# Kernel tuning notes

Hardware: AMD Instinct MI355X
Metric: run time of the kernel (lower is better)

Reference implementation:

```python
import jax, jax.numpy as jnp
import numpy as np

# Graph sizes
B, N, E = 8, 512, 262144          # graphs, nodes/graph, total edges
ND, ED, GD = 128, 64, 32          # node, edge, glob feature dims
FIN = 2 * ND + ED                 # 320 = msg('sr') + existing edges
CTX = GD                          # ctxt_dim = 0, ctxt is globs only
H1, OUT = 256, 64                 # feat_net hidden / output (== ED for 'add' residual)
AH, NHEADS = 64, 4                # attn_net hidden / heads
HEAD = OUT // NHEADS              # 16
EPS = 1e-5


def setup_inputs() -> dict:
    key = jax.random.key(0)
    ks = jax.random.split(key, 12)
    nodes = jax.random.normal(ks[0], (B, N, ND), jnp.float32)
    edges0 = jax.random.normal(ks[1], (E, ED), jnp.float32)
    globs = jax.random.normal(ks[2], (B, GD), jnp.float32)
    batch_idx = jnp.sort(jax.random.randint(ks[3], (E,), 0, B, jnp.int32))
    send_idx = jax.random.randint(ks[4], (E,), 0, N, jnp.int32)
    recv_idx = jax.random.randint(ks[5], (E,), 0, N, jnp.int32)
    # LayerNorm params over feat_inpt_dim
    ln_g = jnp.ones((FIN,), jnp.float32)
    ln_b = jnp.zeros((FIN,), jnp.float32)
    # feat_net: 2-layer SiLU MLP, ctxt concatenated at the input
    W1 = 0.05 * jax.random.normal(ks[6], (FIN + CTX, H1), jnp.float32)
    b1 = jnp.zeros((H1,), jnp.float32)
    W2 = 0.05 * jax.random.normal(ks[7], (H1, OUT), jnp.float32)
    b2 = jnp.zeros((OUT,), jnp.float32)
    # attn_net: 2-layer SiLU MLP -> n_heads scores
    A1 = 0.05 * jax.random.normal(ks[8], (FIN + CTX, AH), jnp.float32)
    ab1 = jnp.zeros((AH,), jnp.float32)
    A2 = 0.05 * jax.random.normal(ks[9], (AH, NHEADS), jnp.float32)
    ab2 = jnp.zeros((NHEADS,), jnp.float32)
    return dict(nodes=nodes, edges0=edges0, globs=globs, ln_g=ln_g, ln_b=ln_b,
                W1=W1, b1=b1, W2=W2, b2=b2, A1=A1, ab1=ab1, A2=A2, ab2=ab2,
                batch_idx=batch_idx, send_idx=send_idx, recv_idx=recv_idx)


def reference(nodes, edges0, globs, ln_g, ln_b, W1, b1, W2, b2, A1, ab1, A2, ab2,
              batch_idx, send_idx, recv_idx):
    # Build messages: gather sender/receiver node feats per edge ('sr')
    send = nodes[batch_idx, send_idx]                      # [E, ND]
    recv = nodes[batch_idx, recv_idx]                      # [E, ND]
    feats = jnp.concatenate([edges0, send, recv], axis=-1)  # [E, FIN]
    # Pre-LN
    mu = feats.mean(-1, keepdims=True)
    var = feats.var(-1, keepdims=True)
    feats = (feats - mu) * jax.lax.rsqrt(var + EPS) * ln_g + ln_b
    # Broadcast per-graph globals to edges (ctxt_from_mask)
    x = jnp.concatenate([feats, globs[batch_idx]], axis=-1)  # [E, FIN+CTX]
    # Attention scores / sqrt(feat_outp_dim)
    a = (jax.nn.silu(x @ A1 + ab1) @ A2 + ab2) / np.sqrt(OUT)  # [E, NHEADS]
    # Segment softmax over the sender dim (group by (graph, receiver))
    seg = batch_idx * N + recv_idx
    nseg = B * N
    amax = jax.ops.segment_max(a, seg, num_segments=nseg)
    amax = jnp.where(jnp.isfinite(amax), amax, 0.0)
    ae = jnp.exp(a - amax[seg])
    denom = jax.ops.segment_sum(ae, seg, num_segments=nseg)
    attn = ae / denom[seg]                                  # [E, NHEADS]
    attn = jnp.repeat(attn, HEAD, axis=-1)                  # [E, OUT]
    # Edge feature update + additive residual
    new_edges = jax.nn.silu(x @ W1 + b1) @ W2 + b2 + edges0  # [E, OUT]
    # Attention-weighted scatter-sum pool over senders, zeros for isolated nodes
    pooled = jax.ops.segment_sum(new_edges * attn, seg, num_segments=nseg)
    pooled = pooled.reshape(B, N, OUT)
    return new_edges, pooled
```

## Files before the change

kernel.cpp:

```cpp
#include <hip/hip_runtime.h>
#include <hip/hip_bf16.h>
#include <cstdint>

typedef __bf16 bf16;
typedef __bf16 bf16x8 __attribute__((ext_vector_type(8)));
typedef float f32x4 __attribute__((ext_vector_type(4)));
typedef unsigned int u32;

#define E_TOT   262144
#define NNODE   512
#define NDIM    128
#define EDIM    64
#define GDIM    32
#define FIN     320
#define XD      352
#define H1D     256
#define OUTD    64
#define AHD     64
#define NHEADS  4
#define NSEG    4096
#define TE      48
#define CAP     192

#define SX_STR  360
#define SH_STR  264
#define SA_STR  72

#define PRM_LNG 0
#define PRM_LNB 320
#define PRM_B1  640
#define PRM_B2  896
#define PRM_A2  960
#define PRM_AB1 1216
#define PRM_AB2 1280
#define PRM_TOT 1284

#define SMEM_SX    0
#define SMEM_SA    25600
#define SMEM_A2    34560
#define SMEM_LNG   35584
#define SMEM_LNB   36864
#define SMEM_IDX   38144
#define SMEM_TOT   38720

#define SOFF 510

__device__ __forceinline__ float siluf(float v) {
    return v / (1.0f + __expf(-v));
}

__device__ __forceinline__ float ldf(const void* p, size_t i, bool isb) {
    return isb ? (float)((const bf16*)p)[i] : ((const float*)p)[i];
}

__device__ __forceinline__ bool probe_bf16(const void* nodes, int t) {
    const unsigned short* u16 = (const unsigned short*)nodes;
    int lane = t & 63;
    int pl = 0;
    #pragma unroll
    for (int i = 0; i < 4; i++) {
        unsigned short u = u16[lane * 4 + i];
        int expo = (u >> 7) & 0xFF;
        pl += (((u & 0x7FFF) == 0) || (expo >= 97 && expo <= 137)) ? 1 : 0;
    }
    #pragma unroll
    for (int m = 1; m < 64; m <<= 1) pl += __shfl_xor(pl, m);
    return pl >= 240;
}

__global__ __launch_bounds__(256) void k_prep(
    const void* __restrict__ nodes,
    const void* __restrict__ W1, const void* __restrict__ W2, const void* __restrict__ A1,
    const void* __restrict__ ln_g, const void* __restrict__ ln_b,
    const void* __restrict__ b1, const void* __restrict__ b2,
    const void* __restrict__ A2, const void* __restrict__ ab1, const void* __restrict__ ab2,
    const int* __restrict__ bidx, const int* __restrict__ ridx,
    bf16* __restrict__ W1T, bf16* __restrict__ W2T, bf16* __restrict__ A1T,
    float* __restrict__ prm, u32* __restrict__ cnt, u32* __restrict__ order) {
    int b = blockIdx.x, t = threadIdx.x;
    if (b >= SOFF) {
        int ge = (b - SOFF) * 256 + t;
        int seg = bidx[ge] * NNODE + ridx[ge];
        u32 pos = atomicAdd(&cnt[seg], 1u);
        if (pos < CAP) order[(size_t)seg * CAP + pos] = (u32)ge;
        return;
    }
    bool isb = probe_bf16(nodes, t);
    if (b < 352) {
        int i = b * 256 + t;
        int k = i / H1D, n = i % H1D;
        float v = isb ? (float)((const bf16*)W1)[i] : ((const float*)W1)[i];
        W1T[n * XD + k] = (bf16)v;
    } else if (b < 416) {
        int i = (b - 352) * 256 + t;
        int k = i / OUTD, n = i % OUTD;
        float v = isb ? (float)((const bf16*)W2)[i] : ((const float*)W2)[i];
        W2T[n * H1D + k] = (bf16)v;
    } else if (b < 504) {
        int i = (b - 416) * 256 + t;
        int k = i / AHD, n = i % AHD;
        float v = isb ? (float)((const bf16*)A1)[i] : ((const float*)A1)[i];
        A1T[n * XD + k] = (bf16)v;
    } else {
        int i = (b - 504) * 256 + t;
        if (i < PRM_TOT) {
            const void* src; int off;
            if (i < 320)       { src = ln_g; off = i; }
            else if (i < 640)  { src = ln_b; off = i - 320; }
            else if (i < 896)  { src = b1;   off = i - 640; }
            else if (i < 960)  { src = b2;   off = i - 896; }
            else if (i < 1216) { src = A2;   off = i - 960; }
            else if (i < 1280) { src = ab1;  off = i - 1216; }
            else               { src = ab2;  off = i - 1280; }
            prm[i] = isb ? (float)((const bf16*)src)[off] : ((const float*)src)[off];
        }
    }
}

__global__ __launch_bounds__(256, 4) void k_edge(
    const void* __restrict__ nodes, const void* __restrict__ edges0,
    const void* __restrict__ globs, const float* __restrict__ prm,
    const int* __restrict__ bidx, const int* __restrict__ sidx,
    const int* __restrict__ ridx,
    const bf16* __restrict__ W1T, const bf16* __restrict__ W2T,
    const bf16* __restrict__ A1T,
    void* __restrict__ outNE, float* __restrict__ scrS) {

    __shared__ __align__(16) char smem[SMEM_TOT];
    bf16*  sX    = (bf16*)(smem + SMEM_SX);
    bf16*  sH    = (bf16*)(smem + SMEM_SX);
    bf16*  sA    = (bf16*)(smem + SMEM_SA);
    float* sA2   = (float*)(smem + SMEM_A2);
    float* sLnG  = (float*)(smem + SMEM_LNG);
    float* sLnB  = (float*)(smem + SMEM_LNB);
    int*   sBi   = (int*)(smem + SMEM_IDX);
    int*   sSi   = sBi + TE;
    int*   sRi   = sBi + 2 * TE;

    const int t  = threadIdx.x;
    const int e0 = blockIdx.x * TE;
    const int ne = min(TE, E_TOT - e0);
    const bool isb = probe_bf16(nodes, t);

    if (t < TE) {
        int ge = e0 + t;
        if (t < ne) {
            sBi[t] = bidx[ge]; sSi[t] = sidx[ge]; sRi[t] = ridx[ge];
        } else {
            sBi[t] = 0; sSi[t] = 0; sRi[t] = 0;
        }
    } else if (t < 128) {
        int c = t - 48;
        if (c < 80) ((float4*)sLnG)[c] = ((const float4*)(prm + PRM_LNG))[c];
    } else if (t < 208) {
        int c = t - 128;
        ((float4*)sLnB)[c] = ((const float4*)(prm + PRM_LNB))[c];
    } else {
        int c = t - 208;
        if (c < 32) {
            ((float4*)sA2)[c]      = ((const float4*)(prm + PRM_A2))[c];
            ((float4*)sA2)[c + 32] = ((const float4*)(prm + PRM_A2))[c + 32];
        }
    }
    __syncthreads();

    {
        const int eh = t >> 3, gl = t & 7;
        for (int half = 0; half < 2; half++) {
            const int e = half * 32 + eh;
            if (e >= TE) break;
            if (e >= ne) {
                bf16x8 zz = {};
                #pragma unroll
                for (int j = 0; j < 6; j++) {
                    int c = gl + j * 8;
                    if (c < 44) *(bf16x8*)&sX[e * SX_STR + c * 8] = zz;
                }
                continue;
            }
            const int ge = e0 + e;
            const int bi = sBi[e], si = sSi[e], ri = sRi[e];
            float v[40];
            #pragma unroll
            for (int j = 0; j < 5; j++) {
                const int c = gl + j * 8;
                const void* base; size_t off;
                if (c < 8)       { base = edges0; off = (size_t)ge * EDIM + c * 8; }
                else if (c < 24) { base = nodes;  off = (size_t)(bi * NNODE + si) * NDIM + (c - 8) * 8; }
                else             { base = nodes;  off = (size_t)(bi * NNODE + ri) * NDIM + (c - 24) * 8; }
                if (isb) {
                    bf16x8 x = *(const bf16x8*)((const bf16*)base + off);
                    #pragma unroll
                    for (int ii = 0; ii < 8; ii++) v[j * 8 + ii] = (float)x[ii];
                } else {
                    const float* sf = (const float*)base + off;
                    float4 f0 = ((const float4*)sf)[0];
                    float4 f1 = ((const float4*)sf)[1];
                    v[j*8+0]=f0.x; v[j*8+1]=f0.y; v[j*8+2]=f0.z; v[j*8+3]=f0.w;
                    v[j*8+4]=f1.x; v[j*8+5]=f1.y; v[j*8+6]=f1.z; v[j*8+7]=f1.w;
                }
            }
            float s = 0.f, sq = 0.f;
            #pragma unroll
            for (int ii = 0; ii < 40; ii++) { s += v[ii]; sq += v[ii] * v[ii]; }
            #pragma unroll
            for (int m = 1; m < 8; m <<= 1) { s += __shfl_xor(s, m); sq += __shfl_xor(sq, m); }
            float mean = s * (1.0f / FIN);
            float var  = sq * (1.0f / FIN) - mean * mean;
            float rstd = rsqrtf(var + 1e-5f);
            #pragma unroll
            for (int j = 0; j < 5; j++) {
                const int c = gl + j * 8;
                const float* gP = &sLnG[c * 8];
                const float* bP = &sLnB[c * 8];
                bf16x8 o;
                #pragma unroll
                for (int ii = 0; ii < 8; ii++)
                    o[ii] = (bf16)((v[j * 8 + ii] - mean) * rstd * gP[ii] + bP[ii]);
                *(bf16x8*)&sX[e * SX_STR + c * 8] = o;
            }
            if (gl < 4) {
                const int c = 40 + gl;
                size_t off = (size_t)bi * GDIM + gl * 8;
                bf16x8 o;
                if (isb) {
                    o = *(const bf16x8*)((const bf16*)globs + off);
                } else {
                    const float* sf = (const float*)globs + off;
                    float4 f0 = ((const float4*)sf)[0];
                    float4 f1 = ((const float4*)sf)[1];
                    o[0]=(bf16)f0.x; o[1]=(bf16)f0.y; o[2]=(bf16)f0.z; o[3]=(bf16)f0.w;
                    o[4]=(bf16)f1.x; o[5]=(bf16)f1.y; o[6]=(bf16)f1.z; o[7]=(bf16)f1.w;
                }
                *(bf16x8*)&sX[e * SX_STR + c * 8] = o;
            }
        }
    }
    __syncthreads();

    const int w = t >> 6, lane = t & 63, quad = lane >> 4, l15 = lane & 15;
    f32x4 z = {0.f, 0.f, 0.f, 0.f};

    f32x4 acc[3][4], accA[3];
    #pragma unroll
    for (int s2 = 0; s2 < 3; s2++) { accA[s2] = z; for (int i = 0; i < 4; i++) acc[s2][i] = z; }
    {
        const bf16* pW = W1T + (size_t)(w * 64 + l15) * XD + quad * 8;
        const bf16* pA = A1T + (size_t)(w * 16 + l15) * XD + quad * 8;
        bf16x8 bw[4], ba;
        #pragma unroll
        for (int i = 0; i < 4; i++) bw[i] = *(const bf16x8*)(pW + (size_t)i * 16 * XD);
        ba = *(const bf16x8*)pA;
        #pragma unroll 1
        for (int kk = 0; kk < 11; kk++) {
            bf16x8 bwn[4], ban;
            if (kk < 10) {
                #pragma unroll
                for (int i = 0; i < 4; i++) bwn[i] = *(const bf16x8*)(pW + (size_t)i * 16 * XD + (kk + 1) * 32);
                ban = *(const bf16x8*)(pA + (kk + 1) * 32);
            }
            const int kc = kk * 32 + quad * 8;
            bf16x8 a[3];
            #pragma unroll
            for (int s2 = 0; s2 < 3; s2++) a[s2] = *(bf16x8*)&sX[(s2 * 16 + l15) * SX_STR + kc];
            #pragma unroll
            for (int i = 0; i < 4; i++)
                #pragma unroll
                for (int s2 = 0; s2 < 3; s2++)
                    acc[s2][i] = __builtin_amdgcn_mfma_f32_16x16x32_bf16(a[s2], bw[i], acc[s2][i], 0, 0, 0);
            #pragma unroll
            for (int s2 = 0; s2 < 3; s2++)
                accA[s2] = __builtin_amdgcn_mfma_f32_16x16x32_bf16(a[s2], ba, accA[s2], 0, 0, 0);
            if (kk < 10) {
                #pragma unroll
                for (int i = 0; i < 4; i++) bw[i] = bwn[i];
                ba = ban;
            }
        }
    }
    __syncthreads();

    #pragma unroll
    for (int i = 0; i < 4; i++) {
        const int n = w * 64 + i * 16 + l15;
        const float bb = prm[PRM_B1 + n];
        #pragma unroll
        for (int s2 = 0; s2 < 3; s2++)
            #pragma unroll
            for (int r = 0; r < 4; r++)
                sH[(s2 * 16 + quad * 4 + r) * SH_STR + n] = (bf16)siluf(acc[s2][i][r] + bb);
    }
    {
        const int n = w * 16 + l15;
        const float ba1 = prm[PRM_AB1 + n];
        #pragma unroll
        for (int s2 = 0; s2 < 3; s2++)
            #pragma unroll
            for (int r = 0; r < 4; r++)
                sA[(s2 * 16 + quad * 4 + r) * SA_STR + n] = (bf16)siluf(accA[s2][r] + ba1);
    }
    __syncthreads();

    if (t < TE * NHEADS) {
        const int e = t >> 2, h = t & 3;
        if (e < ne) {
            float dot = 0.f;
            #pragma unroll
            for (int c = 0; c < 8; c++) {
                bf16x8 vv = *(bf16x8*)&sA[e * SA_STR + c * 8];
                #pragma unroll
                for (int ii = 0; ii < 8; ii++)
                    dot += (float)vv[ii] * sA2[(c * 8 + ii) * NHEADS + h];
            }
            scrS[(size_t)(e0 + e) * NHEADS + h] = __expf((dot + prm[PRM_AB2 + h]) * 0.125f);
        }
    }

    {
        f32x4 c2[3] = {z, z, z};
        const int n = w * 16 + l15;
        const bf16* pW2 = W2T + (size_t)n * H1D + quad * 8;
        bf16x8 b2f = *(const bf16x8*)pW2;
        #pragma unroll 1
        for (int kk = 0; kk < 8; kk++) {
            bf16x8 b2n;
            if (kk < 7) b2n = *(const bf16x8*)(pW2 + (kk + 1) * 32);
            const int kc = kk * 32 + quad * 8;
            #pragma unroll
            for (int s2 = 0; s2 < 3; s2++) {
                bf16x8 a = *(bf16x8*)&sH[(s2 * 16 + l15) * SH_STR + kc];
                c2[s2] = __builtin_amdgcn_mfma_f32_16x16x32_bf16(a, b2f, c2[s2], 0, 0, 0);
            }
            if (kk < 7) b2f = b2n;
        }
        const float bb2 = prm[PRM_B2 + n];
        #pragma unroll
        for (int s2 = 0; s2 < 3; s2++)
            #pragma unroll
            for (int r = 0; r < 4; r++) {
                const int row = s2 * 16 + quad * 4 + r;
                if (row < ne) {
                    size_t off = (size_t)(e0 + row) * EDIM + n;
                    float ev = isb ? (float)((const bf16*)edges0)[off] : ((const float*)edges0)[off];
                    float v = c2[s2][r] + bb2 + ev;
                    if (isb) ((bf16*)outNE)[off] = (bf16)v;
                    else     ((float*)outNE)[off] = v;
                }
            }
    }
}

__global__ __launch_bounds__(256) void k_pool(const u32* __restrict__ cnt,
                                              const u32* __restrict__ order,
                                              const float* __restrict__ scrS,
                                              const void* __restrict__ nodes,
                                              void* __restrict__ d_out) {
    const int t = threadIdx.x;
    const bool isb = probe_bf16(nodes, t);
    const int ws = blockIdx.x * 4 + (t >> 6);
    const int lane = t & 63, h = lane >> 4;
    const void* newE = d_out;

    const u32 n1 = min(cnt[ws], (u32)CAP);
    const u32 base = (u32)ws * CAP;
    float acc = 0.f, dsum = 0.f;
    u32 i = 0;
    for (; i + 4 <= n1; i += 4) {
        u32 ea = order[base + i], eb = order[base + i + 1];
        u32 ec = order[base + i + 2], ed = order[base + i + 3];
        float sa = scrS[(size_t)ea * NHEADS + h];
        float sb = scrS[(size_t)eb * NHEADS + h];
        float sc = scrS[(size_t)ec * NHEADS + h];
        float sd = scrS[(size_t)ed * NHEADS + h];
        float va = ldf(newE, (size_t)ea * EDIM + lane, isb);
        float vb = ldf(newE, (size_t)eb * EDIM + lane, isb);
        float vc = ldf(newE, (size_t)ec * EDIM + lane, isb);
        float vd = ldf(newE, (size_t)ed * EDIM + lane, isb);
        acc += va * sa + vb * sb + vc * sc + vd * sd;
        dsum += sa + sb + sc + sd;
    }
    for (; i < n1; i++) {
        u32 e = order[base + i];
        float s = scrS[(size_t)e * NHEADS + h];
        acc += ldf(newE, (size_t)e * EDIM + lane, isb) * s;
        dsum += s;
    }
    float r = (dsum > 0.f) ? acc / dsum : 0.f;
    size_t po = (size_t)E_TOT * OUTD + (size_t)ws * OUTD + lane;
    if (isb) ((bf16*)d_out)[po] = (bf16)r;
    else     ((float*)d_out)[po] = r;
}

static char* align_up(char* p, size_t a) {
    return (char*)(((uintptr_t)p + (a - 1)) & ~(uintptr_t)(a - 1));
}

extern "C" void kernel_launch(void* const* d_in, const int* in_sizes, int n_in,
                              void* d_out, int out_size, void* d_ws, size_t ws_size,
                              hipStream_t stream) {
    const void* nodes  = d_in[0];
    const void* edges0 = d_in[1];
    const void* globs  = d_in[2];
    const void* ln_g   = d_in[3];
    const void* ln_b   = d_in[4];
    const void* W1     = d_in[5];
    const void* b1     = d_in[6];
    const void* W2     = d_in[7];
    const void* b2     = d_in[8];
    const void* A1     = d_in[9];
    const void* ab1    = d_in[10];
    const void* A2     = d_in[11];
    const void* ab2    = d_in[12];
    const int*  bidx   = (const int*)d_in[13];
    const int*  sidx   = (const int*)d_in[14];
    const int*  ridx   = (const int*)d_in[15];

    char* p = (char*)d_ws;
    float* prm    = (float*)p;  p = align_up(p + PRM_TOT * 4, 256);
    bf16*  W1T    = (bf16*)p;   p = align_up(p + XD * H1D * 2, 256);
    bf16*  W2T    = (bf16*)p;   p = align_up(p + H1D * OUTD * 2, 256);
    bf16*  A1T    = (bf16*)p;   p = align_up(p + XD * AHD * 2, 256);
    u32*   cnt    = (u32*)p;    p += NSEG * 4;
    u32*   order  = (u32*)p;    p += (size_t)NSEG * CAP * 4;
    float* scrS   = (float*)p;  p += (size_t)E_TOT * NHEADS * 4;

    hipMemsetAsync(cnt, 0, NSEG * 4, stream);
    k_prep<<<dim3(SOFF + E_TOT / 256), dim3(256), 0, stream>>>(
        nodes, W1, W2, A1, ln_g, ln_b, b1, b2, A2, ab1, ab2,
        bidx, ridx, W1T, W2T, A1T, prm, cnt, order);
    k_edge<<<dim3((E_TOT + TE - 1) / TE), dim3(256), 0, stream>>>(
        nodes, edges0, globs, prm,
        bidx, sidx, ridx, W1T, W2T, A1T, d_out, scrS);
    k_pool<<<dim3(NSEG / 4), dim3(256), 0, stream>>>(cnt, order, scrS, nodes, d_out);
}
```

Before: 333.0 us.

## Precompute per-node and per-graph first-layer projections, folding LayerNorm algebraically

The per-edge first layer (K=352) is factored by linearity. LayerNorm is folded into the weights as rstd*(x·gW - mu*sum(gW)) + ln_b·W. The sender, receiver and global contributions are precomputed once per node and per graph in k_prep, along with per-node sum and sum-of-squares stats. The edge kernel then runs MFMA only over the 64 edge features and adds gathered fp32 table rows. This removes most of the per-edge GEMM work and the node-feature gathers, at the cost of large fp32 table gathers (4096x256 per table) per edge row, a heavier prep kernel, and numerical differences from the mean-subtraction reformulation.

```diff
diff --git a/kernel.cpp b/kernel.cpp
--- a/kernel.cpp
+++ b/kernel.cpp
@@ -13,18 +13,17 @@
 #define EDIM    64
 #define GDIM    32
 #define FIN     320
-#define XD      352
 #define H1D     256
 #define OUTD    64
 #define AHD     64
 #define NHEADS  4
 #define NSEG    4096
+#define NND     4096
 #define TE      48
 #define CAP     192
 
-#define SX_STR  360
+#define SX_STR  72
 #define SH_STR  264
-#define SA_STR  72
 
 #define PRM_LNG 0
 #define PRM_LNB 320
@@ -35,15 +34,23 @@
 #define PRM_AB2 1280
 #define PRM_TOT 1284
 
-#define SMEM_SX    0
-#define SMEM_SA    25600
-#define SMEM_A2    34560
-#define SMEM_LNG   35584
-#define SMEM_LNB   36864
-#define SMEM_IDX   38144
-#define SMEM_TOT   38720
-
-#define SOFF 510
+#define SMEM_SH    0
+#define SMEM_SX    25600
+#define SMEM_MU    32512
+#define SMEM_A2    32896
+#define SMEM_IDX   33920
+#define SMEM_TOT   34496
+
+#define KP_W1E   0
+#define KP_A1E   64
+#define KP_W2T   80
+#define KP_PRM   144
+#define KP_GL    150
+#define KP_GC    158
+#define KP_GCA   159
+#define KP_TAB   160
+#define KP_SCAT  672
+#define KP_NBLK  1696
 
 __device__ __forceinline__ float siluf(float v) {
     return v / (1.0f + __expf(-v));
@@ -69,40 +76,48 @@
 }
 
 __global__ __launch_bounds__(256) void k_prep(
-    const void* __restrict__ nodes,
+    const void* __restrict__ nodes, const void* __restrict__ globs,
     const void* __restrict__ W1, const void* __restrict__ W2, const void* __restrict__ A1,
     const void* __restrict__ ln_g, const void* __restrict__ ln_b,
     const void* __restrict__ b1, const void* __restrict__ b2,
     const void* __restrict__ A2, const void* __restrict__ ab1, const void* __restrict__ ab2,
     const int* __restrict__ bidx, const int* __restrict__ ridx,
-    bf16* __restrict__ W1T, bf16* __restrict__ W2T, bf16* __restrict__ A1T,
-    float* __restrict__ prm, u32* __restrict__ cnt, u32* __restrict__ order) {
+    bf16* __restrict__ W1eT, bf16* __restrict__ A1eT, bf16* __restrict__ W2T,
+    float* __restrict__ prm,
+    float* __restrict__ Gvec, float* __restrict__ Cvec,
+    float* __restrict__ GAv,  float* __restrict__ CAv,
+    float* __restrict__ Gltab, float* __restrict__ GlAtab,
+    float2* __restrict__ SQ,
+    float* __restrict__ Stab, float* __restrict__ Rtab,
+    float* __restrict__ SAtab, float* __restrict__ RAtab,
+    u32* __restrict__ cnt, u32* __restrict__ order) {
+
+    __shared__ float sNd[1024];
     int b = blockIdx.x, t = threadIdx.x;
-    if (b >= SOFF) {
-        int ge = (b - SOFF) * 256 + t;
+
+    if (b >= KP_SCAT) {
+        int ge = (b - KP_SCAT) * 256 + t;
         int seg = bidx[ge] * NNODE + ridx[ge];
         u32 pos = atomicAdd(&cnt[seg], 1u);
         if (pos < CAP) order[(size_t)seg * CAP + pos] = (u32)ge;
         return;
     }
     bool isb = probe_bf16(nodes, t);
-    if (b < 352) {
+
+    if (b < KP_A1E) {
         int i = b * 256 + t;
-        int k = i / H1D, n = i % H1D;
-        float v = isb ? (float)((const bf16*)W1)[i] : ((const float*)W1)[i];
-        W1T[n * XD + k] = (bf16)v;
-    } else if (b < 416) {
-        int i = (b - 352) * 256 + t;
-        int k = i / OUTD, n = i % OUTD;
-        float v = isb ? (float)((const bf16*)W2)[i] : ((const float*)W2)[i];
-        W2T[n * H1D + k] = (bf16)v;
-    } else if (b < 504) {
-        int i = (b - 416) * 256 + t;
-        int k = i / AHD, n = i % AHD;
-        float v = isb ? (float)((const bf16*)A1)[i] : ((const float*)A1)[i];
-        A1T[n * XD + k] = (bf16)v;
-    } else {
-        int i = (b - 504) * 256 + t;
+        int n = i >> 6, k = i & 63;
+        W1eT[i] = (bf16)(ldf(ln_g, k, isb) * ldf(W1, (size_t)k * H1D + n, isb));
+    } else if (b < KP_W2T) {
+        int i = (b - KP_A1E) * 256 + t;
+        int n = i >> 6, k = i & 63;
+        A1eT[i] = (bf16)(ldf(ln_g, k, isb) * ldf(A1, (size_t)k * AHD + n, isb));
+    } else if (b < KP_PRM) {
+        int i = (b - KP_W2T) * 256 + t;
+        int k = i >> 6, n = i & 63;
+        W2T[n * H1D + k] = (bf16)ldf(W2, i, isb);
+    } else if (b < KP_GL) {
+        int i = (b - KP_PRM) * 256 + t;
         if (i < PRM_TOT) {
             const void* src; int off;
             if (i < 320)       { src = ln_g; off = i; }
@@ -112,30 +127,121 @@
             else if (i < 1216) { src = A2;   off = i - 960; }
             else if (i < 1280) { src = ab1;  off = i - 1216; }
             else               { src = ab2;  off = i - 1280; }
-            prm[i] = isb ? (float)((const bf16*)src)[off] : ((const float*)src)[off];
+            prm[i] = ldf(src, off, isb);
+        }
+    } else if (b < KP_GC) {
+        int bg = b - KP_GL;
+        float acc = 0.f;
+        #pragma unroll 4
+        for (int k = 0; k < GDIM; k++)
+            acc += ldf(globs, bg * GDIM + k, isb) * ldf(W1, (size_t)(FIN + k) * H1D + t, isb);
+        Gltab[bg * H1D + t] = acc;
+        if (t < AHD) {
+            float a2 = 0.f;
+            #pragma unroll 4
+            for (int k = 0; k < GDIM; k++)
+                a2 += ldf(globs, bg * GDIM + k, isb) * ldf(A1, (size_t)(FIN + k) * AHD + t, isb);
+            GlAtab[bg * AHD + t] = a2;
+        }
+    } else if (b < KP_GCA) {
+        float g = 0.f, c = ldf(b1, t, isb);
+        #pragma unroll 4
+        for (int k = 0; k < FIN; k++) {
+            float wv = ldf(W1, (size_t)k * H1D + t, isb);
+            g += ldf(ln_g, k, isb) * wv;
+            c += ldf(ln_b, k, isb) * wv;
+        }
+        Gvec[t] = g; Cvec[t] = c;
+    } else if (b < KP_TAB) {
+        if (t < AHD) {
+            float g = 0.f, c = ldf(ab1, t, isb);
+            #pragma unroll 4
+            for (int k = 0; k < FIN; k++) {
+                float wv = ldf(A1, (size_t)k * AHD + t, isb);
+                g += ldf(ln_g, k, isb) * wv;
+                c += ldf(ln_b, k, isb) * wv;
+            }
+            GAv[t] = g; CAv[t] = c;
+        }
+    } else {
+        int v0 = (b - KP_TAB) * 8;
+        #pragma unroll
+        for (int q = 0; q < 4; q++)
+            sNd[t + q * 256] = ldf(nodes, (size_t)v0 * NDIM + t + q * 256, isb);
+        __syncthreads();
+        {
+            int nj = t >> 5, li = t & 31;
+            float s = 0.f, qq = 0.f;
+            #pragma unroll
+            for (int m = 0; m < 4; m++) {
+                float x = sNd[nj * NDIM + li + m * 32];
+                s += x; qq += x * x;
+            }
+            #pragma unroll
+            for (int m = 1; m < 32; m <<= 1) { s += __shfl_xor(s, m); qq += __shfl_xor(qq, m); }
+            if (li == 0) SQ[v0 + nj] = make_float2(s, qq);
+        }
+        {
+            float aS[8] = {}, aR[8] = {};
+            for (int k = 0; k < NDIM; k++) {
+                float wS = ldf(ln_g, EDIM + k, isb) * ldf(W1, (size_t)(EDIM + k) * H1D + t, isb);
+                float wR = ldf(ln_g, EDIM + NDIM + k, isb) * ldf(W1, (size_t)(EDIM + NDIM + k) * H1D + t, isb);
+                #pragma unroll
+                for (int j = 0; j < 8; j++) {
+                    aS[j] += sNd[j * NDIM + k] * wS;
+                    aR[j] += sNd[j * NDIM + k] * wR;
+                }
+            }
+            #pragma unroll
+            for (int j = 0; j < 8; j++) {
+                Stab[(size_t)(v0 + j) * H1D + t] = aS[j];
+                Rtab[(size_t)(v0 + j) * H1D + t] = aR[j];
+            }
+        }
+        if (t < AHD) {
+            float aS[8] = {}, aR[8] = {};
+            for (int k = 0; k < NDIM; k++) {
+                float wS = ldf(ln_g, EDIM + k, isb) * ldf(A1, (size_t)(EDIM + k) * AHD + t, isb);
+                float wR = ldf(ln_g, EDIM + NDIM + k, isb) * ldf(A1, (size_t)(EDIM + NDIM + k) * AHD + t, isb);
+                #pragma unroll
+                for (int j = 0; j < 8; j++) {
+                    aS[j] += sNd[j * NDIM + k] * wS;
+                    aR[j] += sNd[j * NDIM + k] * wR;
+                }
+            }
+            #pragma unroll
+            for (int j = 0; j < 8; j++) {
+                SAtab[(size_t)(v0 + j) * AHD + t] = aS[j];
+                RAtab[(size_t)(v0 + j) * AHD + t] = aR[j];
+            }
         }
     }
 }
 
 __global__ __launch_bounds__(256, 4) void k_edge(
     const void* __restrict__ nodes, const void* __restrict__ edges0,
-    const void* __restrict__ globs, const float* __restrict__ prm,
+    const float* __restrict__ prm,
     const int* __restrict__ bidx, const int* __restrict__ sidx,
     const int* __restrict__ ridx,
-    const bf16* __restrict__ W1T, const bf16* __restrict__ W2T,
-    const bf16* __restrict__ A1T,
+    const bf16* __restrict__ W1eT, const bf16* __restrict__ A1eT,
+    const bf16* __restrict__ W2T,
+    const float* __restrict__ Gvec, const float* __restrict__ Cvec,
+    const float* __restrict__ GAv,  const float* __restrict__ CAv,
+    const float* __restrict__ Gltab, const float* __restrict__ GlAtab,
+    const float2* __restrict__ SQ,
+    const float* __restrict__ Stab, const float* __restrict__ Rtab,
+    const float* __restrict__ SAtab, const float* __restrict__ RAtab,
     void* __restrict__ outNE, float* __restrict__ scrS) {
 
     __shared__ __align__(16) char smem[SMEM_TOT];
-    bf16*  sX    = (bf16*)(smem + SMEM_SX);
-    bf16*  sH    = (bf16*)(smem + SMEM_SX);
-    bf16*  sA    = (bf16*)(smem + SMEM_SA);
-    float* sA2   = (float*)(smem + SMEM_A2);
-    float* sLnG  = (float*)(smem + SMEM_LNG);
-    float* sLnB  = (float*)(smem + SMEM_LNB);
-    int*   sBi   = (int*)(smem + SMEM_IDX);
-    int*   sSi   = sBi + TE;
-    int*   sRi   = sBi + 2 * TE;
+    bf16*   sH   = (bf16*)(smem + SMEM_SH);
+    bf16*   sX   = (bf16*)(smem + SMEM_SX);
+    bf16*   sA   = (bf16*)(smem + SMEM_SX);
+    float2* sMu  = (float2*)(smem + SMEM_MU);
+    float*  sA2  = (float*)(smem + SMEM_A2);
+    int*    sBi  = (int*)(smem + SMEM_IDX);
+    int*    sNs  = sBi + TE;
+    int*    sNr  = sBi + 2 * TE;
 
     const int t  = threadIdx.x;
     const int e0 = blockIdx.x * TE;
@@ -144,23 +250,14 @@
 
     if (t < TE) {
         int ge = e0 + t;
-        if (t < ne) {
-            sBi[t] = bidx[ge]; sSi[t] = sidx[ge]; sRi[t] = ridx[ge];
-        } else {
-            sBi[t] = 0; sSi[t] = 0; sRi[t] = 0;
-        }
-    } else if (t < 128) {
-        int c = t - 48;
-        if (c < 80) ((float4*)sLnG)[c] = ((const float4*)(prm + PRM_LNG))[c];
-    } else if (t < 208) {
-        int c = t - 128;
-        ((float4*)sLnB)[c] = ((const float4*)(prm + PRM_LNB))[c];
-    } else {
-        int c = t - 208;
-        if (c < 32) {
-            ((float4*)sA2)[c]      = ((const float4*)(prm + PRM_A2))[c];
-            ((float4*)sA2)[c + 32] = ((const float4*)(prm + PRM_A2))[c + 32];
-        }
+        int bi = 0, si = 0, ri = 0;
+        if (t < ne) { bi = bidx[ge]; si = sidx[ge]; ri = ridx[ge]; }
+        int ns = bi * NNODE + si, nr = bi * NNODE + ri;
+        sBi[t] = bi; sNs[t] = ns; sNr[t] = nr;
+        float2 a = SQ[ns], c = SQ[nr];
+        sMu[t] = make_float2(a.x + c.x, a.y + c.y);
+    } else if (t >= 64 && t < 128) {
+        ((float4*)sA2)[t - 64] = ((const float4*)(prm + PRM_A2))[t - 64];
     }
     __syncthreads();
 
@@ -171,68 +268,38 @@
             if (e >= TE) break;
             if (e >= ne) {
                 bf16x8 zz = {};
+                *(bf16x8*)&sX[e * SX_STR + gl * 8] = zz;
+                if (gl == 0) sMu[e] = make_float2(0.f, 1.f);
+                continue;
+            }
+            const size_t off = (size_t)(e0 + e) * EDIM + gl * 8;
+            float v[8];
+            bf16x8 o;
+            if (isb) {
+                o = *(const bf16x8*)((const bf16*)edges0 + off);
                 #pragma unroll
-                for (int j = 0; j < 6; j++) {
-                    int c = gl + j * 8;
-                    if (c < 44) *(bf16x8*)&sX[e * SX_STR + c * 8] = zz;
-                }
-                continue;
-            }
-            const int ge = e0 + e;
-            const int bi = sBi[e], si = sSi[e], ri = sRi[e];
-            float v[40];
-            #pragma unroll
-            for (int j = 0; j < 5; j++) {
-                const int c = gl + j * 8;
-                const void* base; size_t off;
-                if (c < 8)       { base = edges0; off = (size_t)ge * EDIM + c * 8; }
-                else if (c < 24) { base = nodes;  off = (size_t)(bi * NNODE + si) * NDIM + (c - 8) * 8; }
-                else             { base = nodes;  off = (size_t)(bi * NNODE + ri) * NDIM + (c - 24) * 8; }
-                if (isb) {
-                    bf16x8 x = *(const bf16x8*)((const bf16*)base + off);
-                    #pragma unroll
-                    for (int ii = 0; ii < 8; ii++) v[j * 8 + ii] = (float)x[ii];
-                } else {
-                    const float* sf = (const float*)base + off;
-                    float4 f0 = ((const float4*)sf)[0];
-                    float4 f1 = ((const float4*)sf)[1];
-                    v[j*8+0]=f0.x; v[j*8+1]=f0.y; v[j*8+2]=f0.z; v[j*8+3]=f0.w;
-                    v[j*8+4]=f1.x; v[j*8+5]=f1.y; v[j*8+6]=f1.z; v[j*8+7]=f1.w;
-                }
-            }
+                for (int ii = 0; ii < 8; ii++) v[ii] = (float)o[ii];
+            } else {
+                const float* sf = (const float*)edges0 + off;
+                float4 f0 = ((const float4*)sf)[0];
+                float4 f1 = ((const float4*)sf)[1];
+                v[0]=f0.x; v[1]=f0.y; v[2]=f0.z; v[3]=f0.w;
+                v[4]=f1.x; v[5]=f1.y; v[6]=f1.z; v[7]=f1.w;
+                #pragma unroll
+                for (int ii = 0; ii < 8; ii++) o[ii] = (bf16)v[ii];
+            }
+            *(bf16x8*)&sX[e * SX_STR + gl * 8] = o;
             float s = 0.f, sq = 0.f;
             #pragma unroll
-            for (int ii = 0; ii < 40; ii++) { s += v[ii]; sq += v[ii] * v[ii]; }
+            for (int ii = 0; ii < 8; ii++) { s += v[ii]; sq += v[ii] * v[ii]; }
             #pragma unroll
             for (int m = 1; m < 8; m <<= 1) { s += __shfl_xor(s, m); sq += __shfl_xor(sq, m); }
-            float mean = s * (1.0f / FIN);
-            float var  = sq * (1.0f / FIN) - mean * mean;
-            float rstd = rsqrtf(var + 1e-5f);
-            #pragma unroll
-            for (int j = 0; j < 5; j++) {
-                const int c = gl + j * 8;
-                const float* gP = &sLnG[c * 8];
-                const float* bP = &sLnB[c * 8];
-                bf16x8 o;
-                #pragma unroll
-                for (int ii = 0; ii < 8; ii++)
-                    o[ii] = (bf16)((v[j * 8 + ii] - mean) * rstd * gP[ii] + bP[ii]);
-                *(bf16x8*)&sX[e * SX_STR + c * 8] = o;
-            }
-            if (gl < 4) {
-                const int c = 40 + gl;
-                size_t off = (size_t)bi * GDIM + gl * 8;
-                bf16x8 o;
-                if (isb) {
-                    o = *(const bf16x8*)((const bf16*)globs + off);
-                } else {
-                    const float* sf = (const float*)globs + off;
-                    float4 f0 = ((const float4*)sf)[0];
-                    float4 f1 = ((const float4*)sf)[1];
-                    o[0]=(bf16)f0.x; o[1]=(bf16)f0.y; o[2]=(bf16)f0.z; o[3]=(bf16)f0.w;
-                    o[4]=(bf16)f1.x; o[5]=(bf16)f1.y; o[6]=(bf16)f1.z; o[7]=(bf16)f1.w;
-                }
-                *(bf16x8*)&sX[e * SX_STR + c * 8] = o;
+            if (gl == 0) {
+                float2 nq = sMu[e];
+                float st = s + nq.x, qt = sq + nq.y;
+                float mean = st * (1.0f / FIN);
+                float var  = qt * (1.0f / FIN) - mean * mean;
+                sMu[e] = make_float2(mean, rsqrtf(var + 1e-5f));
             }
         }
     }
@@ -245,20 +312,14 @@
     #pragma unroll
     for (int s2 = 0; s2 < 3; s2++) { accA[s2] = z; for (int i = 0; i < 4; i++) acc[s2][i] = z; }
     {
-        const bf16* pW = W1T + (size_t)(w * 64 + l15) * XD + quad * 8;
-        const bf16* pA = A1T + (size_t)(w * 16 + l15) * XD + quad * 8;
-        bf16x8 bw[4], ba;
+        const bf16* pW = W1eT + (size_t)(w * 64 + l15) * EDIM + quad * 8;
+        const bf16* pA = A1eT + (size_t)(w * 16 + l15) * EDIM + quad * 8;
         #pragma unroll
-        for (int i = 0; i < 4; i++) bw[i] = *(const bf16x8*)(pW + (size_t)i * 16 * XD);
-        ba = *(const bf16x8*)pA;
-        #pragma unroll 1
-        for (int kk = 0; kk < 11; kk++) {
-            bf16x8 bwn[4], ban;
-            if (kk < 10) {
-                #pragma unroll
-                for (int i = 0; i < 4; i++) bwn[i] = *(const bf16x8*)(pW + (size_t)i * 16 * XD + (kk + 1) * 32);
-                ban = *(const bf16x8*)(pA + (kk + 1) * 32);
-            }
+        for (int kk = 0; kk < 2; kk++) {
+            bf16x8 bw[4], ba;
+            #pragma unroll
+            for (int i = 0; i < 4; i++) bw[i] = *(const bf16x8*)(pW + i * 16 * EDIM + kk * 32);
+            ba = *(const bf16x8*)(pA + kk * 32);
             const int kc = kk * 32 + quad * 8;
             bf16x8 a[3];
             #pragma unroll
@@ -271,33 +332,38 @@
             #pragma unroll
             for (int s2 = 0; s2 < 3; s2++)
                 accA[s2] = __builtin_amdgcn_mfma_f32_16x16x32_bf16(a[s2], ba, accA[s2], 0, 0, 0);
-            if (kk < 10) {
-                #pragma unroll
-                for (int i = 0; i < 4; i++) bw[i] = bwn[i];
-                ba = ban;
-            }
         }
     }
     __syncthreads();
 
-    #pragma unroll
+    #pragma unroll 1
     for (int i = 0; i < 4; i++) {
         const int n = w * 64 + i * 16 + l15;
-        const float bb = prm[PRM_B1 + n];
+        const float Gn = Gvec[n], Cn = Cvec[n];
         #pragma unroll
         for (int s2 = 0; s2 < 3; s2++)
             #pragma unroll
-            for (int r = 0; r < 4; r++)
-                sH[(s2 * 16 + quad * 4 + r) * SH_STR + n] = (bf16)siluf(acc[s2][i][r] + bb);
+            for (int r = 0; r < 4; r++) {
+                const int row = s2 * 16 + quad * 4 + r;
+                float2 mr = sMu[row];
+                float S = Stab[(size_t)sNs[row] * H1D + n] + Rtab[(size_t)sNr[row] * H1D + n];
+                float val = mr.y * (acc[s2][i][r] + S - mr.x * Gn) + Gltab[sBi[row] * H1D + n] + Cn;
+                sH[row * SH_STR + n] = (bf16)siluf(val);
+            }
     }
     {
         const int n = w * 16 + l15;
-        const float ba1 = prm[PRM_AB1 + n];
+        const float Gn = GAv[n], Cn = CAv[n];
         #pragma unroll
         for (int s2 = 0; s2 < 3; s2++)
             #pragma unroll
-            for (int r = 0; r < 4; r++)
-                sA[(s2 * 16 + quad * 4 + r) * SA_STR + n] = (bf16)siluf(accA[s2][r] + ba1);
+            for (int r = 0; r < 4; r++) {
+                const int row = s2 * 16 + quad * 4 + r;
+                float2 mr = sMu[row];
+                float S = SAtab[(size_t)sNs[row] * AHD + n] + RAtab[(size_t)sNr[row] * AHD + n];
+                float val = mr.y * (accA[s2][r] + S - mr.x * Gn) + GlAtab[sBi[row] * AHD + n] + Cn;
+                sA[row * SX_STR + n] = (bf16)siluf(val);
+            }
     }
     __syncthreads();
 
@@ -307,7 +373,7 @@
             float dot = 0.f;
             #pragma unroll
             for (int c = 0; c < 8; c++) {
-                bf16x8 vv = *(bf16x8*)&sA[e * SA_STR + c * 8];
+                bf16x8 vv = *(bf16x8*)&sA[e * SX_STR + c * 8];
                 #pragma unroll
                 for (int ii = 0; ii < 8; ii++)
                     dot += (float)vv[ii] * sA2[(c * 8 + ii) * NHEADS + h];
@@ -416,20 +482,34 @@
     const int*  ridx   = (const int*)d_in[15];
 
     char* p = (char*)d_ws;
-    float* prm    = (float*)p;  p = align_up(p + PRM_TOT * 4, 256);
-    bf16*  W1T    = (bf16*)p;   p = align_up(p + XD * H1D * 2, 256);
-    bf16*  W2T    = (bf16*)p;   p = align_up(p + H1D * OUTD * 2, 256);
-    bf16*  A1T    = (bf16*)p;   p = align_up(p + XD * AHD * 2, 256);
-    u32*   cnt    = (u32*)p;    p += NSEG * 4;
-    u32*   order  = (u32*)p;    p += (size_t)NSEG * CAP * 4;
-    float* scrS   = (float*)p;  p += (size_t)E_TOT * NHEADS * 4;
+    float*  prm    = (float*)p;   p = align_up(p + PRM_TOT * 4, 256);
+    bf16*   W1eT   = (bf16*)p;    p = align_up(p + H1D * EDIM * 2, 256);
+    bf16*   A1eT   = (bf16*)p;    p = align_up(p + AHD * EDIM * 2, 256);
+    bf16*   W2T    = (bf16*)p;    p = align_up(p + H1D * OUTD * 2, 256);
+    float*  Gvec   = (float*)p;   p += H1D * 4;
+    float*  Cvec   = (float*)p;   p += H1D * 4;
+    float*  GAv    = (float*)p;   p += AHD * 4;
+    float*  CAv    = (float*)p;   p += AHD * 4;
+    float*  Gltab  = (float*)p;   p += 8 * H1D * 4;
+    float*  GlAtab = (float*)p;   p = align_up(p + 8 * AHD * 4, 256);
+    float2* SQ     = (float2*)p;  p += (size_t)NND * 8;
+    float*  Stab   = (float*)p;   p += (size_t)NND * H1D * 4;
+    float*  Rtab   = (float*)p;   p += (size_t)NND * H1D * 4;
+    float*  SAtab  = (float*)p;   p += (size_t)NND * AHD * 4;
+    float*  RAtab  = (float*)p;   p += (size_t)NND * AHD * 4;
+    u32*    cnt    = (u32*)p;     p += NSEG * 4;
+    u32*    order  = (u32*)p;     p += (size_t)NSEG * CAP * 4;
+    float*  scrS   = (float*)p;   p += (size_t)E_TOT * NHEADS * 4;
 
     hipMemsetAsync(cnt, 0, NSEG * 4, stream);
-    k_prep<<<dim3(SOFF + E_TOT / 256), dim3(256), 0, stream>>>(
-        nodes, W1, W2, A1, ln_g, ln_b, b1, b2, A2, ab1, ab2,
-        bidx, ridx, W1T, W2T, A1T, prm, cnt, order);
+    k_prep<<<dim3(KP_NBLK), dim3(256), 0, stream>>>(
+        nodes, globs, W1, W2, A1, ln_g, ln_b, b1, b2, A2, ab1, ab2,
+        bidx, ridx, W1eT, A1eT, W2T, prm,
+        Gvec, Cvec, GAv, CAv, Gltab, GlAtab, SQ,
+        Stab, Rtab, SAtab, RAtab, cnt, order);
     k_edge<<<dim3((E_TOT + TE - 1) / TE), dim3(256), 0, stream>>>(
-        nodes, edges0, globs, prm,
-        bidx, sidx, ridx, W1T, W2T, A1T, d_out, scrS);
+        nodes, edges0, prm, bidx, sidx, ridx,
+        W1eT, A1eT, W2T, Gvec, Cvec, GAv, CAv, Gltab, GlAtab, SQ,
+        Stab, Rtab, SAtab, RAtab, d_out, scrS);
     k_pool<<<dim3(NSEG / 4), dim3(256), 0, stream>>>(cnt, order, scrS, nodes, d_out);
 }
```

Measured after the change: 576.7 us. 1.73x slower.

## Fold LayerNorm affine and normalization into GEMM epilogue via precomputed weight sums

Applied to the files above, without the earlier changes.

Precomputes gamma-scaled W1/A1 and per-output vectors G=gamma·W and C=beta·W+bias in the prep kernel. The edge kernel stores raw (unnormalized) features in shared memory and applies rstd*acc - rstd*mean*G + C in the epilogue, and scales globs by the std so they stay unnormalized. This removes per-element LayerNorm arithmetic and the ln param staging from the gather phase. Rounding raw values to bf16 before mean subtraction adds a precision risk, and the prep kernel gains atomics.

```diff
diff --git a/kernel.cpp b/kernel.cpp
--- a/kernel.cpp
+++ b/kernel.cpp
@@ -36,14 +36,19 @@
 #define PRM_TOT 1284
 
 #define SMEM_SX    0
+#define SMEM_A2    34560
+#define SMEM_IDX   35584
+#define SMEM_MU    36160
+#define SMEM_TOT   36544
 #define SMEM_SA    25600
-#define SMEM_A2    34560
-#define SMEM_LNG   35584
-#define SMEM_LNB   36864
-#define SMEM_IDX   38144
-#define SMEM_TOT   38720
-
-#define SOFF 510
+
+#define KP_W1T   0
+#define KP_W2T   352
+#define KP_A1T   416
+#define KP_PRM   504
+#define KP_GC    510
+#define KP_SCAT  550
+#define KP_NBLK  1574
 
 __device__ __forceinline__ float siluf(float v) {
     return v / (1.0f + __expf(-v));
@@ -76,33 +81,34 @@
     const void* __restrict__ A2, const void* __restrict__ ab1, const void* __restrict__ ab2,
     const int* __restrict__ bidx, const int* __restrict__ ridx,
     bf16* __restrict__ W1T, bf16* __restrict__ W2T, bf16* __restrict__ A1T,
-    float* __restrict__ prm, u32* __restrict__ cnt, u32* __restrict__ order) {
+    float* __restrict__ prm,
+    float* __restrict__ Gvec, float* __restrict__ Cvec,
+    float* __restrict__ GAv,  float* __restrict__ CAv,
+    u32* __restrict__ cnt, u32* __restrict__ order) {
     int b = blockIdx.x, t = threadIdx.x;
-    if (b >= SOFF) {
-        int ge = (b - SOFF) * 256 + t;
+    if (b >= KP_SCAT) {
+        int ge = (b - KP_SCAT) * 256 + t;
         int seg = bidx[ge] * NNODE + ridx[ge];
         u32 pos = atomicAdd(&cnt[seg], 1u);
         if (pos < CAP) order[(size_t)seg * CAP + pos] = (u32)ge;
         return;
     }
     bool isb = probe_bf16(nodes, t);
-    if (b < 352) {
-        int i = b * 256 + t;
-        int k = i / H1D, n = i % H1D;
-        float v = isb ? (float)((const bf16*)W1)[i] : ((const float*)W1)[i];
-        W1T[n * XD + k] = (bf16)v;
-    } else if (b < 416) {
-        int i = (b - 352) * 256 + t;
+    if (b < KP_W2T) {
+        int k = b, n = t;
+        float g = (k < FIN) ? ldf(ln_g, k, isb) : 1.0f;
+        W1T[n * XD + k] = (bf16)(ldf(W1, (size_t)k * H1D + n, isb) * g);
+    } else if (b < KP_A1T) {
+        int i = (b - KP_W2T) * 256 + t;
         int k = i / OUTD, n = i % OUTD;
-        float v = isb ? (float)((const bf16*)W2)[i] : ((const float*)W2)[i];
-        W2T[n * H1D + k] = (bf16)v;
-    } else if (b < 504) {
-        int i = (b - 416) * 256 + t;
-        int k = i / AHD, n = i % AHD;
-        float v = isb ? (float)((const bf16*)A1)[i] : ((const float*)A1)[i];
-        A1T[n * XD + k] = (bf16)v;
-    } else {
-        int i = (b - 504) * 256 + t;
+        W2T[n * H1D + k] = (bf16)ldf(W2, i, isb);
+    } else if (b < KP_PRM) {
+        int i = (b - KP_A1T) * 256 + t;
+        int k = i >> 6, n = i & 63;
+        float g = (k < FIN) ? ldf(ln_g, k, isb) : 1.0f;
+        A1T[n * XD + k] = (bf16)(ldf(A1, i, isb) * g);
+    } else if (b < KP_GC) {
+        int i = (b - KP_PRM) * 256 + t;
         if (i < PRM_TOT) {
             const void* src; int off;
             if (i < 320)       { src = ln_g; off = i; }
@@ -112,7 +118,33 @@
             else if (i < 1216) { src = A2;   off = i - 960; }
             else if (i < 1280) { src = ab1;  off = i - 1216; }
             else               { src = ab2;  off = i - 1280; }
-            prm[i] = isb ? (float)((const bf16*)src)[off] : ((const float*)src)[off];
+            prm[i] = ldf(src, off, isb);
+        }
+    } else {
+        int j = b - KP_GC;
+        float g = 0.f, c = 0.f;
+        #pragma unroll
+        for (int kk = 0; kk < 8; kk++) {
+            int k = j * 8 + kk;
+            float gam = ldf(ln_g, k, isb), bet = ldf(ln_b, k, isb);
+            float wv = ldf(W1, (size_t)k * H1D + t, isb);
+            g += gam * wv; c += bet * wv;
+        }
+        if (j == 0) c += ldf(b1, t, isb);
+        atomicAdd(&Gvec[t], g);
+        atomicAdd(&Cvec[t], c);
+        if (t < AHD) {
+            float gA = 0.f, cA = 0.f;
+            #pragma unroll
+            for (int kk = 0; kk < 8; kk++) {
+                int k = j * 8 + kk;
+                float wv = ldf(A1, (size_t)k * AHD + t, isb);
+                gA += ldf(ln_g, k, isb) * wv;
+                cA += ldf(ln_b, k, isb) * wv;
+            }
+            if (j == 0) cA += ldf(ab1, t, isb);
+            atomicAdd(&GAv[t], gA);
+            atomicAdd(&CAv[t], cA);
         }
     }
 }
@@ -124,18 +156,19 @@
     const int* __restrict__ ridx,
     const bf16* __restrict__ W1T, const bf16* __restrict__ W2T,
     const bf16* __restrict__ A1T,
+    const float* __restrict__ Gvec, const float* __restrict__ Cvec,
+    const float* __restrict__ GAv,  const float* __restrict__ CAv,
     void* __restrict__ outNE, float* __restrict__ scrS) {
 
     __shared__ __align__(16) char smem[SMEM_TOT];
-    bf16*  sX    = (bf16*)(smem + SMEM_SX);
-    bf16*  sH    = (bf16*)(smem + SMEM_SX);
-    bf16*  sA    = (bf16*)(smem + SMEM_SA);
-    float* sA2   = (float*)(smem + SMEM_A2);
-    float* sLnG  = (float*)(smem + SMEM_LNG);
-    float* sLnB  = (float*)(smem + SMEM_LNB);
-    int*   sBi   = (int*)(smem + SMEM_IDX);
-    int*   sSi   = sBi + TE;
-    int*   sRi   = sBi + 2 * TE;
+    bf16*   sX   = (bf16*)(smem + SMEM_SX);
+    bf16*   sH   = (bf16*)(smem + SMEM_SX);
+    bf16*   sA   = (bf16*)(smem + SMEM_SA);
+    float*  sA2  = (float*)(smem + SMEM_A2);
+    int*    sBi  = (int*)(smem + SMEM_IDX);
+    int*    sSi  = sBi + TE;
+    int*    sRi  = sBi + 2 * TE;
+    float2* sMu  = (float2*)(smem + SMEM_MU);
 
     const int t  = threadIdx.x;
     const int e0 = blockIdx.x * TE;
@@ -149,18 +182,8 @@
         } else {
             sBi[t] = 0; sSi[t] = 0; sRi[t] = 0;
         }
-    } else if (t < 128) {
-        int c = t - 48;
-        if (c < 80) ((float4*)sLnG)[c] = ((const float4*)(prm + PRM_LNG))[c];
-    } else if (t < 208) {
-        int c = t - 128;
-        ((float4*)sLnB)[c] = ((const float4*)(prm + PRM_LNB))[c];
-    } else {
-        int c = t - 208;
-        if (c < 32) {
-            ((float4*)sA2)[c]      = ((const float4*)(prm + PRM_A2))[c];
-            ((float4*)sA2)[c + 32] = ((const float4*)(prm + PRM_A2))[c + 32];
-        }
+    } else if (t >= 64 && t < 128) {
+        ((float4*)sA2)[t - 64] = ((const float4*)(prm + PRM_A2))[t - 64];
     }
     __syncthreads();
 
@@ -176,11 +199,13 @@
                     int c = gl + j * 8;
                     if (c < 44) *(bf16x8*)&sX[e * SX_STR + c * 8] = zz;
                 }
+                if (gl == 0) sMu[e] = make_float2(1.f, 0.f);
                 continue;
             }
             const int ge = e0 + e;
             const int bi = sBi[e], si = sSi[e], ri = sRi[e];
             float v[40];
+            bf16x8 xr[5];
             #pragma unroll
             for (int j = 0; j < 5; j++) {
                 const int c = gl + j * 8;
@@ -189,15 +214,17 @@
                 else if (c < 24) { base = nodes;  off = (size_t)(bi * NNODE + si) * NDIM + (c - 8) * 8; }
                 else             { base = nodes;  off = (size_t)(bi * NNODE + ri) * NDIM + (c - 24) * 8; }
                 if (isb) {
-                    bf16x8 x = *(const bf16x8*)((const bf16*)base + off);
+                    xr[j] = *(const bf16x8*)((const bf16*)base + off);
                     #pragma unroll
-                    for (int ii = 0; ii < 8; ii++) v[j * 8 + ii] = (float)x[ii];
+                    for (int ii = 0; ii < 8; ii++) v[j * 8 + ii] = (float)xr[j][ii];
                 } else {
                     const float* sf = (const float*)base + off;
                     float4 f0 = ((const float4*)sf)[0];
                     float4 f1 = ((const float4*)sf)[1];
                     v[j*8+0]=f0.x; v[j*8+1]=f0.y; v[j*8+2]=f0.z; v[j*8+3]=f0.w;
                     v[j*8+4]=f1.x; v[j*8+5]=f1.y; v[j*8+6]=f1.z; v[j*8+7]=f1.w;
+                    #pragma unroll
+                    for (int ii = 0; ii < 8; ii++) xr[j][ii] = (bf16)v[j * 8 + ii];
                 }
             }
             float s = 0.f, sq = 0.f;
@@ -208,29 +235,27 @@
             float mean = s * (1.0f / FIN);
             float var  = sq * (1.0f / FIN) - mean * mean;
             float rstd = rsqrtf(var + 1e-5f);
+            float sd   = (var + 1e-5f) * rstd;
+            if (gl == 0) sMu[e] = make_float2(rstd, -rstd * mean);
             #pragma unroll
             for (int j = 0; j < 5; j++) {
                 const int c = gl + j * 8;
-                const float* gP = &sLnG[c * 8];
-                const float* bP = &sLnB[c * 8];
-                bf16x8 o;
-                #pragma unroll
-                for (int ii = 0; ii < 8; ii++)
-                    o[ii] = (bf16)((v[j * 8 + ii] - mean) * rstd * gP[ii] + bP[ii]);
-                *(bf16x8*)&sX[e * SX_STR + c * 8] = o;
+                *(bf16x8*)&sX[e * SX_STR + c * 8] = xr[j];
             }
             if (gl < 4) {
                 const int c = 40 + gl;
                 size_t off = (size_t)bi * GDIM + gl * 8;
                 bf16x8 o;
                 if (isb) {
-                    o = *(const bf16x8*)((const bf16*)globs + off);
+                    bf16x8 gr = *(const bf16x8*)((const bf16*)globs + off);
+                    #pragma unroll
+                    for (int ii = 0; ii < 8; ii++) o[ii] = (bf16)((float)gr[ii] * sd);
                 } else {
                     const float* sf = (const float*)globs + off;
                     float4 f0 = ((const float4*)sf)[0];
                     float4 f1 = ((const float4*)sf)[1];
-                    o[0]=(bf16)f0.x; o[1]=(bf16)f0.y; o[2]=(bf16)f0.z; o[3]=(bf16)f0.w;
-                    o[4]=(bf16)f1.x; o[5]=(bf16)f1.y; o[6]=(bf16)f1.z; o[7]=(bf16)f1.w;
+                    o[0]=(bf16)(f0.x*sd); o[1]=(bf16)(f0.y*sd); o[2]=(bf16)(f0.z*sd); o[3]=(bf16)(f0.w*sd);
+                    o[4]=(bf16)(f1.x*sd); o[5]=(bf16)(f1.y*sd); o[6]=(bf16)(f1.z*sd); o[7]=(bf16)(f1.w*sd);
                 }
                 *(bf16x8*)&sX[e * SX_STR + c * 8] = o;
             }
@@ -280,24 +305,32 @@
     }
     __syncthreads();
 
-    #pragma unroll
+    #pragma unroll 1
     for (int i = 0; i < 4; i++) {
         const int n = w * 64 + i * 16 + l15;
-        const float bb = prm[PRM_B1 + n];
+        const float Gn = Gvec[n], Cn = Cvec[n];
         #pragma unroll
         for (int s2 = 0; s2 < 3; s2++)
             #pragma unroll
-            for (int r = 0; r < 4; r++)
-                sH[(s2 * 16 + quad * 4 + r) * SH_STR + n] = (bf16)siluf(acc[s2][i][r] + bb);
+            for (int r = 0; r < 4; r++) {
+                const int row = s2 * 16 + quad * 4 + r;
+                float2 mr = sMu[row];
+                float val = mr.x * acc[s2][i][r] + mr.y * Gn + Cn;
+                sH[row * SH_STR + n] = (bf16)siluf(val);
+            }
     }
     {
         const int n = w * 16 + l15;
-        const float ba1 = prm[PRM_AB1 + n];
+        const float Gn = GAv[n], Cn = CAv[n];
         #pragma unroll
         for (int s2 = 0; s2 < 3; s2++)
             #pragma unroll
-            for (int r = 0; r < 4; r++)
-                sA[(s2 * 16 + quad * 4 + r) * SA_STR + n] = (bf16)siluf(accA[s2][r] + ba1);
+            for (int r = 0; r < 4; r++) {
+                const int row = s2 * 16 + quad * 4 + r;
+                float2 mr = sMu[row];
+                float val = mr.x * accA[s2][r] + mr.y * Gn + Cn;
+                sA[row * SA_STR + n] = (bf16)siluf(val);
+            }
     }
     __syncthreads();
 
@@ -421,15 +454,19 @@
     bf16*  W2T    = (bf16*)p;   p = align_up(p + H1D * OUTD * 2, 256);
     bf16*  A1T    = (bf16*)p;   p = align_up(p + XD * AHD * 2, 256);
     u32*   cnt    = (u32*)p;    p += NSEG * 4;
+    float* Gvec   = (float*)p;  p += H1D * 4;
+    float* Cvec   = (float*)p;  p += H1D * 4;
+    float* GAv    = (float*)p;  p += AHD * 4;
+    float* CAv    = (float*)p;  p = align_up(p + AHD * 4, 256);
     u32*   order  = (u32*)p;    p += (size_t)NSEG * CAP * 4;
     float* scrS   = (float*)p;  p += (size_t)E_TOT * NHEADS * 4;
 
-    hipMemsetAsync(cnt, 0, NSEG * 4, stream);
-    k_prep<<<dim3(SOFF + E_TOT / 256), dim3(256), 0, stream>>>(
+    hipMemsetAsync(cnt, 0, NSEG * 4 + (H1D + H1D + AHD + AHD) * 4, stream);
+    k_prep<<<dim3(KP_NBLK), dim3(256), 0, stream>>>(
         nodes, W1, W2, A1, ln_g, ln_b, b1, b2, A2, ab1, ab2,
-        bidx, ridx, W1T, W2T, A1T, prm, cnt, order);
+        bidx, ridx, W1T, W2T, A1T, prm, Gvec, Cvec, GAv, CAv, cnt, order);
     k_edge<<<dim3((E_TOT + TE - 1) / TE), dim3(256), 0, stream>>>(
-        nodes, edges0, globs, prm,
-        bidx, sidx, ridx, W1T, W2T, A1T, d_out, scrS);
+        nodes, edges0, globs, prm, bidx, sidx, ridx,
+        W1T, W2T, A1T, Gvec, Cvec, GAv, CAv, d_out, scrS);
     k_pool<<<dim3(NSEG / 4), dim3(256), 0, stream>>>(cnt, order, scrS, nodes, d_out);
 }
```

Result: slower. 418.6 us (+25.7%).

## Move segment bucketing into edge kernel and zero counters inside prep kernel

Applied to the files above, without the earlier changes.

The per-edge atomic bucketing of edges into (graph, receiver) segments moves out of the prep kernel's extra 1024 blocks and into the tail of the edge kernel, reusing the batch and receiver indices already staged in shared memory. The separate hipMemsetAsync on the counters is replaced by one extra prep block that zeroes them with vector stores. This removes one launch and a redundant global read of the index arrays. In exchange the atomics now sit at the end of the compute-heavy edge kernel, and the order within each segment bucket may differ.

```diff
diff --git a/kernel.cpp b/kernel.cpp
--- a/kernel.cpp
+++ b/kernel.cpp
@@ -43,7 +43,7 @@
 #define SMEM_IDX   38144
 #define SMEM_TOT   38720
 
-#define SOFF 510
+#define KP_NBLK  511
 
 __device__ __forceinline__ float siluf(float v) {
     return v / (1.0f + __expf(-v));
@@ -74,33 +74,28 @@
     const void* __restrict__ ln_g, const void* __restrict__ ln_b,
     const void* __restrict__ b1, const void* __restrict__ b2,
     const void* __restrict__ A2, const void* __restrict__ ab1, const void* __restrict__ ab2,
-    const int* __restrict__ bidx, const int* __restrict__ ridx,
     bf16* __restrict__ W1T, bf16* __restrict__ W2T, bf16* __restrict__ A1T,
-    float* __restrict__ prm, u32* __restrict__ cnt, u32* __restrict__ order) {
+    float* __restrict__ prm, u32* __restrict__ cnt) {
     int b = blockIdx.x, t = threadIdx.x;
-    if (b >= SOFF) {
-        int ge = (b - SOFF) * 256 + t;
-        int seg = bidx[ge] * NNODE + ridx[ge];
-        u32 pos = atomicAdd(&cnt[seg], 1u);
-        if (pos < CAP) order[(size_t)seg * CAP + pos] = (u32)ge;
+    if (b == 510) {
+        uint4 z4 = {0u, 0u, 0u, 0u};
+        #pragma unroll
+        for (int q = 0; q < 4; q++) ((uint4*)cnt)[t * 4 + q] = z4;
         return;
     }
     bool isb = probe_bf16(nodes, t);
     if (b < 352) {
         int i = b * 256 + t;
         int k = i / H1D, n = i % H1D;
-        float v = isb ? (float)((const bf16*)W1)[i] : ((const float*)W1)[i];
-        W1T[n * XD + k] = (bf16)v;
+        W1T[n * XD + k] = (bf16)ldf(W1, i, isb);
     } else if (b < 416) {
         int i = (b - 352) * 256 + t;
         int k = i / OUTD, n = i % OUTD;
-        float v = isb ? (float)((const bf16*)W2)[i] : ((const float*)W2)[i];
-        W2T[n * H1D + k] = (bf16)v;
+        W2T[n * H1D + k] = (bf16)ldf(W2, i, isb);
     } else if (b < 504) {
         int i = (b - 416) * 256 + t;
         int k = i / AHD, n = i % AHD;
-        float v = isb ? (float)((const bf16*)A1)[i] : ((const float*)A1)[i];
-        A1T[n * XD + k] = (bf16)v;
+        A1T[n * XD + k] = (bf16)ldf(A1, i, isb);
     } else {
         int i = (b - 504) * 256 + t;
         if (i < PRM_TOT) {
@@ -112,7 +107,7 @@
             else if (i < 1216) { src = A2;   off = i - 960; }
             else if (i < 1280) { src = ab1;  off = i - 1216; }
             else               { src = ab2;  off = i - 1280; }
-            prm[i] = isb ? (float)((const bf16*)src)[off] : ((const float*)src)[off];
+            prm[i] = ldf(src, off, isb);
         }
     }
 }
@@ -124,7 +119,8 @@
     const int* __restrict__ ridx,
     const bf16* __restrict__ W1T, const bf16* __restrict__ W2T,
     const bf16* __restrict__ A1T,
-    void* __restrict__ outNE, float* __restrict__ scrS) {
+    void* __restrict__ outNE, float* __restrict__ scrS,
+    u32* __restrict__ cnt, u32* __restrict__ order) {
 
     __shared__ __align__(16) char smem[SMEM_TOT];
     bf16*  sX    = (bf16*)(smem + SMEM_SX);
@@ -347,6 +343,12 @@
                     else     ((float*)outNE)[off] = v;
                 }
             }
+    }
+
+    if (t < ne) {
+        int seg = sBi[t] * NNODE + sRi[t];
+        u32 pos = atomicAdd(&cnt[seg], 1u);
+        if (pos < CAP) order[(size_t)seg * CAP + pos] = (u32)(e0 + t);
     }
 }
 
@@ -424,12 +426,11 @@
     u32*   order  = (u32*)p;    p += (size_t)NSEG * CAP * 4;
     float* scrS   = (float*)p;  p += (size_t)E_TOT * NHEADS * 4;
 
-    hipMemsetAsync(cnt, 0, NSEG * 4, stream);
-    k_prep<<<dim3(SOFF + E_TOT / 256), dim3(256), 0, stream>>>(
+    k_prep<<<dim3(KP_NBLK), dim3(256), 0, stream>>>(
         nodes, W1, W2, A1, ln_g, ln_b, b1, b2, A2, ab1, ab2,
-        bidx, ridx, W1T, W2T, A1T, prm, cnt, order);
+        W1T, W2T, A1T, prm, cnt);
     k_edge<<<dim3((E_TOT + TE - 1) / TE), dim3(256), 0, stream>>>(
         nodes, edges0, globs, prm,
-        bidx, sidx, ridx, W1T, W2T, A1T, d_out, scrS);
+        bidx, sidx, ridx, W1T, W2T, A1T, d_out, scrS, cnt, order);
     k_pool<<<dim3(NSEG / 4), dim3(256), 0, stream>>>(cnt, order, scrS, nodes, d_out);
 }
```

Result: faster. 318.3 us (-4.4%).
